# Optimization experiments

Measured on AMD Instinct MI355X. Metric: run time of the kernel, lower is better.

## Reference

```python
import jax, jax.numpy as jnp
import numpy as np

N_NODES = 100000
N_EDGES = 1600000
D_IN, D_HID, D_OUT = 128, 128, 64


def setup_inputs() -> dict:
    key = jax.random.key(0)
    ks = jax.random.split(key, 6)
    x = jax.random.normal(ks[0], (N_NODES, D_IN), dtype=jnp.float32)
    edge_index = jax.random.randint(ks[1], (2, N_EDGES), 0, N_NODES, dtype=jnp.int64)
    s1 = 1.0 / np.sqrt(D_IN)
    s2 = 1.0 / np.sqrt(D_HID)
    return {
        "x": x,
        "edge_index": edge_index,
        "Wl1": jax.random.uniform(ks[2], (D_HID, D_IN), jnp.float32, -s1, s1),
        "bl1": jnp.zeros((D_HID,), jnp.float32),
        "Wr1": jax.random.uniform(ks[3], (D_HID, D_IN), jnp.float32, -s1, s1),
        "Wl2": jax.random.uniform(ks[4], (D_OUT, D_HID), jnp.float32, -s2, s2),
        "bl2": jnp.zeros((D_OUT,), jnp.float32),
        "Wr2": jax.random.uniform(ks[5], (D_OUT, D_HID), jnp.float32, -s2, s2),
    }


def _sage_conv(x, src, dst, Wl, bl, Wr, n_nodes):
    # mean-aggregate neighbor features src -> dst
    agg = jax.ops.segment_sum(x[src], dst, num_segments=n_nodes)  # [N, d_in]
    deg = jax.ops.segment_sum(jnp.ones((src.shape[0],), x.dtype), dst, num_segments=n_nodes)
    agg = agg / jnp.maximum(deg, 1.0)[:, None]
    # PyG SAGEConv: lin_l(agg) + lin_r(x), bias only on lin_l
    return agg @ Wl.T + bl + x @ Wr.T


def reference(x, edge_index, Wl1, bl1, Wr1, Wl2, bl2, Wr2):
    src, dst = edge_index[0], edge_index[1]
    n = x.shape[0]
    h = _sage_conv(x, src, dst, Wl1, bl1, Wr1, n)
    h = jax.nn.relu(h)
    # dropout is identity in eval mode (training=False)
    out = _sage_conv(h, src, dst, Wl2, bl2, Wr2, n)
    return out
```

## Files before the change

kernel.cpp:

```cpp
#include <hip/hip_runtime.h>

#define N_NODES_C 100000
#define N_EDGES_C 1600000
#define NT32_C 3125
#define NBUCK_C 392
#define BCAP_C 4800
#define EPB_C 2048

typedef _Float16 half_t;
typedef __attribute__((ext_vector_type(2))) _Float16 half2v;
typedef __attribute__((ext_vector_type(8))) _Float16 half8v;
typedef __attribute__((ext_vector_type(4))) float floatx4;

#if defined(__has_builtin)
#if __has_builtin(__builtin_amdgcn_fdot2)
#define HAS_FDOT2 1
#endif
#endif

__global__ void bucket_kernel(const int* __restrict__ src, const int* __restrict__ dst,
                              int* __restrict__ gcur, int* __restrict__ bucket, int E) {
    __shared__ int lcnt[NBUCK_C];
    __shared__ int lbase[NBUCK_C];
    __shared__ int lcur[NBUCK_C];
    const int tid = threadIdx.x;
    const int e0 = blockIdx.x * EPB_C;
    const int n = min(EPB_C, E - e0);

    for (int i = tid; i < NBUCK_C; i += 256) { lcnt[i] = 0; lcur[i] = 0; }
    __syncthreads();
    for (int i = tid; i < n; i += 256) {
        atomicAdd(&lcnt[dst[e0 + i] >> 8], 1);
    }
    __syncthreads();
    for (int i = tid; i < NBUCK_C; i += 256) {
        int c = lcnt[i];
        lbase[i] = (c > 0) ? atomicAdd(&gcur[i], c) : 0;
    }
    __syncthreads();
    for (int i = tid; i < n; i += 256) {
        int d = dst[e0 + i];
        int s = src[e0 + i];
        int b = d >> 8;
        int p = lbase[b] + atomicAdd(&lcur[b], 1);
        if (p < BCAP_C) bucket[b * BCAP_C + p] = (s << 8) | (d & 255);
    }
}

__global__ void csr_build_kernel(const int* __restrict__ gcur, const int* __restrict__ bucket,
                                 int2* __restrict__ nodeinfo, int* __restrict__ csr, int N) {
    __shared__ int sg[NBUCK_C];
    __shared__ int lcnt[256];
    __shared__ int lcur[256];
    __shared__ int sc[2][256];
    __shared__ int eord[BCAP_C];
    __shared__ int sbase_s;
    const int b = blockIdx.x;
    const int tid = threadIdx.x;
    const int ne = min(gcur[b], BCAP_C);

    for (int i = tid; i < NBUCK_C; i += 256) sg[i] = min(gcur[i], BCAP_C);
    lcnt[tid] = 0;
    lcur[tid] = 0;
    __syncthreads();
    if (tid == 0) {
        int s = 0;
        for (int i = 0; i < b; i++) s += sg[i];
        sbase_s = s;
    }
    const int* be = bucket + b * BCAP_C;
    for (int i = tid; i < ne; i += 256) {
        atomicAdd(&lcnt[be[i] & 255], 1);
    }
    __syncthreads();
    sc[0][tid] = lcnt[tid];
    __syncthreads();
    int cur = 0;
    for (int off = 1; off < 256; off <<= 1) {
        int v = sc[cur][tid] + ((tid >= off) ? sc[cur][tid - off] : 0);
        sc[1 - cur][tid] = v;
        __syncthreads();
        cur ^= 1;
    }
    for (int i = tid; i < ne; i += 256) {
        int p = be[i];
        int dl = p & 255;
        int slot = atomicAdd(&lcur[dl], 1);
        int pre = (dl == 0) ? 0 : sc[cur][dl - 1];
        eord[pre + slot] = p >> 8;
    }
    __syncthreads();
    const int sbase = sbase_s;
    for (int i = tid; i < ne; i += 256) csr[sbase + i] = eord[i];
    int node = (b << 8) + tid;
    if (node < N) {
        int pre = (tid == 0) ? 0 : sc[cur][tid - 1];
        nodeinfo[node] = make_int2(sbase + pre, lcnt[tid]);
    }
}

__global__ void prep_kernel(const float* __restrict__ Wl1, const float* __restrict__ Wr1,
                            const float* __restrict__ Wl2, const float* __restrict__ Wr2,
                            const float* __restrict__ x,
                            half_t* __restrict__ B1, half_t* __restrict__ B2,
                            half_t* __restrict__ xh) {
    int blk = blockIdx.x;
    int tid = threadIdx.x;
    if (blk < 128) {
        int t = blk * 256 + tid;
        int j  = t & 7;
        int l  = (t >> 3) & 63;
        int ks = (t >> 9) & 7;
        int ct = t >> 12;
        int k = ks * 32 + ((l >> 4) << 3) + j;
        int o = ct * 16 + (l & 15);
        float v = (k < 128) ? Wl1[o * 128 + k] : Wr1[o * 128 + (k - 128)];
        B1[t] = (half_t)v;
    } else if (blk < 192) {
        int t = (blk - 128) * 256 + tid;
        int j  = t & 7;
        int l  = (t >> 3) & 63;
        int ks = (t >> 9) & 3;
        int ct = t >> 11;
        int k = ks * 32 + ((l >> 4) << 3) + j;
        int o = ct * 16 + (l & 15);
        float v = (o < 64) ? Wl2[o * 128 + k] : Wr2[(o - 64) * 128 + k];
        B2[t] = (half_t)v;
    } else {
        int t = (blk - 192) * 256 + tid;
        if (t >= N_NODES_C * 16) return;
        const float4* p = (const float4*)x;
        float4 a = p[(size_t)t * 2];
        float4 b = p[(size_t)t * 2 + 1];
        half_t r[8] = {(half_t)a.x, (half_t)a.y, (half_t)a.z, (half_t)a.w,
                       (half_t)b.x, (half_t)b.y, (half_t)b.z, (half_t)b.w};
        *(uint4*)(xh + (size_t)t * 8) = *(uint4*)r;
    }
}

static __device__ __forceinline__ void dot8(float* a, uint4 v) {
    unsigned int u[4] = {v.x, v.y, v.z, v.w};
#ifdef HAS_FDOT2
    const half2v e0 = {(half_t)1.0f, (half_t)0.0f};
    const half2v e1 = {(half_t)0.0f, (half_t)1.0f};
#pragma unroll
    for (int i = 0; i < 4; i++) {
        union { unsigned int x; half2v h; } c; c.x = u[i];
        a[2 * i]     = __builtin_amdgcn_fdot2(c.h, e0, a[2 * i], false);
        a[2 * i + 1] = __builtin_amdgcn_fdot2(c.h, e1, a[2 * i + 1], false);
    }
#else
#pragma unroll
    for (int i = 0; i < 4; i++) {
        union { unsigned int x; half2v h; } c; c.x = u[i];
        a[2 * i]     += (float)c.h.x;
        a[2 * i + 1] += (float)c.h.y;
    }
#endif
}

__launch_bounds__(256, 2)
__global__ void l1_kernel(const half_t* __restrict__ xh,
                          const int2* __restrict__ nodeinfo,
                          const int* __restrict__ csr,
                          const half_t* __restrict__ B1,
                          const float* __restrict__ bias,
                          half_t* __restrict__ hh) {
    __shared__ half_t sA[32][264];

    const int wave = threadIdx.x >> 6;
    const int lane = threadIdx.x & 63;
    const int quad = lane >> 4;
    const int l16 = lane & 15;
    const int tid = threadIdx.x;
    const int node0 = blockIdx.x * 32;

    for (int u = tid; u < 512; u += 256) {
        int n = u >> 4, cc = u & 15;
        *(half8v*)&sA[n][128 + cc * 8] =
            *(const half8v*)(xh + (size_t)(node0 + n) * 128 + cc * 8);
    }

    for (int i = 0; i < 8; i++) {
        const int n = wave * 8 + i;
        const int2 info = nodeinfo[node0 + n];
        const int* row = csr + info.x;
        const int deg = info.y;
        float a0[8] = {0,0,0,0,0,0,0,0};
        float a1[8] = {0,0,0,0,0,0,0,0};
        int e = quad;
        for (; e + 4 < deg; e += 8) {
            int s0 = row[e];
            int s1 = row[e + 4];
            uint4 v0 = *(const uint4*)(xh + (size_t)s0 * 128 + l16 * 8);
            uint4 v1 = *(const uint4*)(xh + (size_t)s1 * 128 + l16 * 8);
            dot8(a0, v0);
            dot8(a1, v1);
        }
        if (e < deg) {
            uint4 v0 = *(const uint4*)(xh + (size_t)row[e] * 128 + l16 * 8);
            dot8(a0, v0);
        }
        float sc = 1.0f / fmaxf((float)deg, 1.0f);
#pragma unroll
        for (int j = 0; j < 8; j++) {
            float v = a0[j] + a1[j];
            v += __shfl_xor(v, 16, 64);
            v += __shfl_xor(v, 32, 64);
            a0[j] = v * sc;
        }
        if (lane < 16) {
            half_t r[8];
#pragma unroll
            for (int j = 0; j < 8; j++) r[j] = (half_t)a0[j];
            *(uint4*)&sA[n][l16 * 8] = *(uint4*)r;
        }
    }
    __syncthreads();

    half8v bf[2][8];
    float bias_v[2];
#pragma unroll
    for (int i = 0; i < 2; i++) {
        int ct = wave * 2 + i;
        bias_v[i] = bias[ct * 16 + l16];
#pragma unroll
        for (int ks = 0; ks < 8; ks++) {
            bf[i][ks] = *(const half8v*)(B1 + ((ct * 8 + ks) * 64 + lane) * 8);
        }
    }

    floatx4 acc[2][2];
#pragma unroll
    for (int i = 0; i < 2; i++)
#pragma unroll
        for (int s = 0; s < 2; s++)
            acc[i][s] = (floatx4){0.f, 0.f, 0.f, 0.f};

#pragma unroll
    for (int ks = 0; ks < 8; ks++) {
        half8v a0 = *(const half8v*)&sA[l16][ks * 32 + quad * 8];
        half8v a1 = *(const half8v*)&sA[16 + l16][ks * 32 + quad * 8];
#pragma unroll
        for (int i = 0; i < 2; i++) {
            acc[i][0] = __builtin_amdgcn_mfma_f32_16x16x32_f16(a0, bf[i][ks], acc[i][0], 0, 0, 0);
            acc[i][1] = __builtin_amdgcn_mfma_f32_16x16x32_f16(a1, bf[i][ks], acc[i][1], 0, 0, 0);
        }
    }

#pragma unroll
    for (int i = 0; i < 2; i++) {
        int o = wave * 32 + i * 16 + l16;
#pragma unroll
        for (int s = 0; s < 2; s++) {
            float vals[4] = {acc[i][s].x, acc[i][s].y, acc[i][s].z, acc[i][s].w};
#pragma unroll
            for (int r = 0; r < 4; r++) {
                int node = node0 + s * 16 + quad * 4 + r;
                float v = fmaxf(vals[r] + bias_v[i], 0.f);
                hh[(size_t)node * 128 + o] = (half_t)v;
            }
        }
    }
}

__launch_bounds__(256, 2)
__global__ void gemm2_kernel(const half_t* __restrict__ hh,
                             const half_t* __restrict__ B2,
                             const float* __restrict__ bias,
                             half_t* __restrict__ g,
                             half_t* __restrict__ s2h) {
    __shared__ half_t sA[32][136];

    const int wave = threadIdx.x >> 6;
    const int lane = threadIdx.x & 63;
    const int quad = lane >> 4;
    const int l16 = lane & 15;

    half8v bf[2][4];
    float bias_v[2];
#pragma unroll
    for (int i = 0; i < 2; i++) {
        int ct = wave * 2 + i;
        int o = ct * 16 + l16;
        bias_v[i] = (o >= 64) ? bias[o - 64] : 0.f;
#pragma unroll
        for (int ks = 0; ks < 4; ks++) {
            bf[i][ks] = *(const half8v*)(B2 + ((ct * 4 + ks) * 64 + lane) * 8);
        }
    }

    const int tid = threadIdx.x;

    for (int tile = blockIdx.x; tile < NT32_C; tile += gridDim.x) {
        const int node0 = tile * 32;
        for (int u = tid; u < 512; u += 256) {
            int n = u >> 4, cc = u & 15;
            *(half8v*)&sA[n][cc * 8] =
                *(const half8v*)(hh + (size_t)(node0 + n) * 128 + cc * 8);
        }
        __syncthreads();

        floatx4 acc[2][2];
#pragma unroll
        for (int i = 0; i < 2; i++)
#pragma unroll
            for (int s = 0; s < 2; s++)
                acc[i][s] = (floatx4){0.f, 0.f, 0.f, 0.f};

#pragma unroll
        for (int ks = 0; ks < 4; ks++) {
            half8v a0 = *(const half8v*)&sA[l16][ks * 32 + quad * 8];
            half8v a1 = *(const half8v*)&sA[16 + l16][ks * 32 + quad * 8];
#pragma unroll
            for (int i = 0; i < 2; i++) {
                acc[i][0] = __builtin_amdgcn_mfma_f32_16x16x32_f16(a0, bf[i][ks], acc[i][0], 0, 0, 0);
                acc[i][1] = __builtin_amdgcn_mfma_f32_16x16x32_f16(a1, bf[i][ks], acc[i][1], 0, 0, 0);
            }
        }

#pragma unroll
        for (int i = 0; i < 2; i++) {
            int o = wave * 32 + i * 16 + l16;
#pragma unroll
            for (int s = 0; s < 2; s++) {
                float vals[4] = {acc[i][s].x, acc[i][s].y, acc[i][s].z, acc[i][s].w};
#pragma unroll
                for (int r = 0; r < 4; r++) {
                    int node = node0 + s * 16 + quad * 4 + r;
                    float v = vals[r] + bias_v[i];
                    if (o < 64) g[(size_t)node * 64 + o] = (half_t)v;
                    else        s2h[(size_t)node * 64 + (o - 64)] = (half_t)v;
                }
            }
        }
        __syncthreads();
    }
}

__global__ void agg2e_kernel(const half_t* __restrict__ g,
                             const half_t* __restrict__ s2h,
                             const int2* __restrict__ nodeinfo,
                             const int* __restrict__ csr,
                             float* __restrict__ out, int N) {
    int wid = (blockIdx.x * 256 + threadIdx.x) >> 6;
    if (wid >= N) return;
    int lane = threadIdx.x & 63;
    int q = lane >> 3;
    int c = lane & 7;
    int2 info = nodeinfo[wid];
    const int* row = csr + info.x;
    const int deg = info.y;
    float a0[8] = {0,0,0,0,0,0,0,0};
    float a1[8] = {0,0,0,0,0,0,0,0};
    int e = q;
    for (; e + 8 < deg; e += 16) {
        int s0 = row[e];
        int s1 = row[e + 8];
        uint4 v0 = *(const uint4*)(g + (size_t)s0 * 64 + c * 8);
        uint4 v1 = *(const uint4*)(g + (size_t)s1 * 64 + c * 8);
        dot8(a0, v0);
        dot8(a1, v1);
    }
    if (e < deg) {
        uint4 v0 = *(const uint4*)(g + (size_t)row[e] * 64 + c * 8);
        dot8(a0, v0);
    }
    float acc[8];
#pragma unroll
    for (int j = 0; j < 8; j++) {
        float v = a0[j] + a1[j];
        v += __shfl_xor(v, 8, 64);
        v += __shfl_xor(v, 16, 64);
        v += __shfl_xor(v, 32, 64);
        acc[j] = v;
    }
    if (lane < 8) {
        float sc = 1.0f / fmaxf((float)deg, 1.0f);
        uint4 sv = *(const uint4*)(s2h + (size_t)wid * 64 + c * 8);
        union { unsigned int x; half2v h; } c0, c1, c2, c3;
        c0.x = sv.x; c1.x = sv.y; c2.x = sv.z; c3.x = sv.w;
        float4 r0, r1;
        r0.x = acc[0] * sc + (float)c0.h.x;
        r0.y = acc[1] * sc + (float)c0.h.y;
        r0.z = acc[2] * sc + (float)c1.h.x;
        r0.w = acc[3] * sc + (float)c1.h.y;
        r1.x = acc[4] * sc + (float)c2.h.x;
        r1.y = acc[5] * sc + (float)c2.h.y;
        r1.z = acc[6] * sc + (float)c3.h.x;
        r1.w = acc[7] * sc + (float)c3.h.y;
        *(float4*)(out + (size_t)wid * 64 + c * 8) = r0;
        *(float4*)(out + (size_t)wid * 64 + c * 8 + 4) = r1;
    }
}

extern "C" void kernel_launch(void* const* d_in, const int* in_sizes, int n_in,
                              void* d_out, int out_size, void* d_ws, size_t ws_size,
                              hipStream_t stream) {
    const float* x    = (const float*)d_in[0];
    const int*   ei   = (const int*)d_in[1];
    const float* Wl1  = (const float*)d_in[2];
    const float* bl1  = (const float*)d_in[3];
    const float* Wr1  = (const float*)d_in[4];
    const float* Wl2  = (const float*)d_in[5];
    const float* bl2  = (const float*)d_in[6];
    const float* Wr2  = (const float*)d_in[7];
    float* out = (float*)d_out;

    const int N = N_NODES_C;
    const int E = N_EDGES_C;
    const int* src = ei;
    const int* dst = ei + E;

    char* ws = (char*)d_ws;
    half_t* B1   = (half_t*)(ws + 0);
    half_t* B2   = (half_t*)(ws + 65536);
    int*    gcur = (int*)   (ws + 98304);
    int2*   nodeinfo = (int2*)(ws + 102400);
    int*    csr  = (int*)   (ws + 1048576);
    half_t* xh   = (half_t*)(ws + 7448576);
    half_t* aggh = (half_t*)(ws + 33048576);
    half_t* hh   = (half_t*)(ws + 58648576);
    half_t* g    = aggh;
    half_t* s2h  = aggh + 6400000;
    int*    bucket = (int*)hh;

    hipMemsetAsync(gcur, 0, NBUCK_C * sizeof(int), stream);
    bucket_kernel<<<(E + EPB_C - 1) / EPB_C, 256, 0, stream>>>(src, dst, gcur, bucket, E);
    csr_build_kernel<<<NBUCK_C, 256, 0, stream>>>(gcur, bucket, nodeinfo, csr, N);

    prep_kernel<<<192 + (N * 16 + 255) / 256, 256, 0, stream>>>(
        Wl1, Wr1, Wl2, Wr2, x, B1, B2, xh);

    l1_kernel<<<NT32_C, 256, 0, stream>>>(xh, nodeinfo, csr, B1, bl1, hh);

    gemm2_kernel<<<512, 256, 0, stream>>>(hh, B2, bl2, g, s2h);
    agg2e_kernel<<<(N + 3) / 4, 256, 0, stream>>>(g, s2h, nodeinfo, csr, out, N);
}
```

Before: 278.7 us.

## Replace bucketed CSR build with global degree count, scan, and atomic scatter

```diff
diff --git a/kernel.cpp b/kernel.cpp
--- a/kernel.cpp
+++ b/kernel.cpp
@@ -4,8 +4,6 @@
 #define N_EDGES_C 1600000
 #define NT32_C 3125
 #define NBUCK_C 392
-#define BCAP_C 4800
-#define EPB_C 2048
 
 typedef _Float16 half_t;
 typedef __attribute__((ext_vector_type(2))) _Float16 half2v;
@@ -18,84 +16,81 @@
 #endif
 #endif
 
-__global__ void bucket_kernel(const int* __restrict__ src, const int* __restrict__ dst,
-                              int* __restrict__ gcur, int* __restrict__ bucket, int E) {
-    __shared__ int lcnt[NBUCK_C];
-    __shared__ int lbase[NBUCK_C];
-    __shared__ int lcur[NBUCK_C];
-    const int tid = threadIdx.x;
-    const int e0 = blockIdx.x * EPB_C;
-    const int n = min(EPB_C, E - e0);
-
-    for (int i = tid; i < NBUCK_C; i += 256) { lcnt[i] = 0; lcur[i] = 0; }
-    __syncthreads();
-    for (int i = tid; i < n; i += 256) {
-        atomicAdd(&lcnt[dst[e0 + i] >> 8], 1);
-    }
-    __syncthreads();
-    for (int i = tid; i < NBUCK_C; i += 256) {
-        int c = lcnt[i];
-        lbase[i] = (c > 0) ? atomicAdd(&gcur[i], c) : 0;
-    }
-    __syncthreads();
-    for (int i = tid; i < n; i += 256) {
-        int d = dst[e0 + i];
-        int s = src[e0 + i];
-        int b = d >> 8;
-        int p = lbase[b] + atomicAdd(&lcur[b], 1);
-        if (p < BCAP_C) bucket[b * BCAP_C + p] = (s << 8) | (d & 255);
-    }
-}
-
-__global__ void csr_build_kernel(const int* __restrict__ gcur, const int* __restrict__ bucket,
-                                 int2* __restrict__ nodeinfo, int* __restrict__ csr, int N) {
-    __shared__ int sg[NBUCK_C];
-    __shared__ int lcnt[256];
-    __shared__ int lcur[256];
+__global__ void deg_kernel(const int* __restrict__ dst, int* __restrict__ deg, int E4) {
+    int t = blockIdx.x * 256 + threadIdx.x;
+    if (t >= E4) return;
+    int4 d = ((const int4*)dst)[t];
+    atomicAdd(&deg[d.x], 1);
+    atomicAdd(&deg[d.y], 1);
+    atomicAdd(&deg[d.z], 1);
+    atomicAdd(&deg[d.w], 1);
+}
+
+__global__ void scan1_kernel(const int* __restrict__ deg, int2* __restrict__ nodeinfo,
+                             int* __restrict__ btot, int N) {
     __shared__ int sc[2][256];
-    __shared__ int eord[BCAP_C];
-    __shared__ int sbase_s;
     const int b = blockIdx.x;
     const int tid = threadIdx.x;
-    const int ne = min(gcur[b], BCAP_C);
-
-    for (int i = tid; i < NBUCK_C; i += 256) sg[i] = min(gcur[i], BCAP_C);
-    lcnt[tid] = 0;
-    lcur[tid] = 0;
-    __syncthreads();
-    if (tid == 0) {
-        int s = 0;
-        for (int i = 0; i < b; i++) s += sg[i];
-        sbase_s = s;
-    }
-    const int* be = bucket + b * BCAP_C;
-    for (int i = tid; i < ne; i += 256) {
-        atomicAdd(&lcnt[be[i] & 255], 1);
-    }
-    __syncthreads();
-    sc[0][tid] = lcnt[tid];
+    const int node = b * 256 + tid;
+    int v = (node < N) ? deg[node] : 0;
+    sc[0][tid] = v;
     __syncthreads();
     int cur = 0;
     for (int off = 1; off < 256; off <<= 1) {
-        int v = sc[cur][tid] + ((tid >= off) ? sc[cur][tid - off] : 0);
-        sc[1 - cur][tid] = v;
+        int nv = sc[cur][tid] + ((tid >= off) ? sc[cur][tid - off] : 0);
+        sc[1 - cur][tid] = nv;
         __syncthreads();
         cur ^= 1;
     }
-    for (int i = tid; i < ne; i += 256) {
-        int p = be[i];
-        int dl = p & 255;
-        int slot = atomicAdd(&lcur[dl], 1);
-        int pre = (dl == 0) ? 0 : sc[cur][dl - 1];
-        eord[pre + slot] = p >> 8;
-    }
+    int incl = sc[cur][tid];
+    if (node < N) nodeinfo[node] = make_int2(incl - v, v);
+    if (tid == 255) btot[b] = incl;
+}
+
+__global__ void scan2_kernel(const int* __restrict__ btot, int* __restrict__ bbase) {
+    __shared__ int sc[2][512];
+    const int tid = threadIdx.x;
+    int v = (tid < NBUCK_C) ? btot[tid] : 0;
+    sc[0][tid] = v;
     __syncthreads();
-    const int sbase = sbase_s;
-    for (int i = tid; i < ne; i += 256) csr[sbase + i] = eord[i];
-    int node = (b << 8) + tid;
-    if (node < N) {
-        int pre = (tid == 0) ? 0 : sc[cur][tid - 1];
-        nodeinfo[node] = make_int2(sbase + pre, lcnt[tid]);
+    int cur = 0;
+    for (int off = 1; off < 512; off <<= 1) {
+        int nv = sc[cur][tid] + ((tid >= off) ? sc[cur][tid - off] : 0);
+        sc[1 - cur][tid] = nv;
+        __syncthreads();
+        cur ^= 1;
+    }
+    if (tid < NBUCK_C) bbase[tid] = sc[cur][tid] - v;
+}
+
+__global__ void fix_kernel(int2* __restrict__ nodeinfo, const int* __restrict__ bbase, int N) {
+    const int b = blockIdx.x;
+    const int node = b * 256 + threadIdx.x;
+    if (node < N) nodeinfo[node].x += bbase[b];
+}
+
+__global__ void scatter_kernel(const int* __restrict__ src, const int* __restrict__ dst,
+                               const int2* __restrict__ nodeinfo, int* __restrict__ cur,
+                               int* __restrict__ csr, int E4) {
+    int t = blockIdx.x * 256 + threadIdx.x;
+    if (t >= E4) return;
+    int4 s = ((const int4*)src)[t];
+    int4 d = ((const int4*)dst)[t];
+    {
+        int p = atomicAdd(&cur[d.x], 1);
+        csr[nodeinfo[d.x].x + p] = s.x;
+    }
+    {
+        int p = atomicAdd(&cur[d.y], 1);
+        csr[nodeinfo[d.y].x + p] = s.y;
+    }
+    {
+        int p = atomicAdd(&cur[d.z], 1);
+        csr[nodeinfo[d.z].x + p] = s.z;
+    }
+    {
+        int p = atomicAdd(&cur[d.w], 1);
+        csr[nodeinfo[d.w].x + p] = s.w;
     }
 }
 
@@ -415,7 +410,8 @@
     char* ws = (char*)d_ws;
     half_t* B1   = (half_t*)(ws + 0);
     half_t* B2   = (half_t*)(ws + 65536);
-    int*    gcur = (int*)   (ws + 98304);
+    int*    btot = (int*)   (ws + 98304);
+    int*    bbase= (int*)   (ws + 100352);
     int2*   nodeinfo = (int2*)(ws + 102400);
     int*    csr  = (int*)   (ws + 1048576);
     half_t* xh   = (half_t*)(ws + 7448576);
@@ -423,11 +419,17 @@
     half_t* hh   = (half_t*)(ws + 58648576);
     half_t* g    = aggh;
     half_t* s2h  = aggh + 6400000;
-    int*    bucket = (int*)hh;
-
-    hipMemsetAsync(gcur, 0, NBUCK_C * sizeof(int), stream);
-    bucket_kernel<<<(E + EPB_C - 1) / EPB_C, 256, 0, stream>>>(src, dst, gcur, bucket, E);
-    csr_build_kernel<<<NBUCK_C, 256, 0, stream>>>(gcur, bucket, nodeinfo, csr, N);
+    int*    deg  = (int*)hh;
+    int*    curp = deg + 100352;
+
+    const int E4 = E / 4;
+
+    hipMemsetAsync(deg, 0, 2 * 100352 * sizeof(int), stream);
+    deg_kernel<<<(E4 + 255) / 256, 256, 0, stream>>>(dst, deg, E4);
+    scan1_kernel<<<NBUCK_C, 256, 0, stream>>>(deg, nodeinfo, btot, N);
+    scan2_kernel<<<1, 512, 0, stream>>>(btot, bbase);
+    fix_kernel<<<NBUCK_C, 256, 0, stream>>>(nodeinfo, bbase, N);
+    scatter_kernel<<<(E4 + 255) / 256, 256, 0, stream>>>(src, dst, nodeinfo, curp, csr, E4);
 
     prep_kernel<<<192 + (N * 16 + 255) / 256, 256, 0, stream>>>(
         Wl1, Wr1, Wl2, Wr2, x, B1, B2, xh);
```

Result: slower. 396.7 us (+42.3%).

## Sort edges locally before bucket scatter and split CSR build across four blocks per bucket

Applied to the files above, without the earlier changes.

```diff
diff --git a/kernel.cpp b/kernel.cpp
--- a/kernel.cpp
+++ b/kernel.cpp
@@ -6,6 +6,7 @@
 #define NBUCK_C 392
 #define BCAP_C 4800
 #define EPB_C 2048
+#define EORD_CAP_C 1536
 
 typedef _Float16 half_t;
 typedef __attribute__((ext_vector_type(2))) _Float16 half2v;
@@ -18,59 +19,100 @@
 #endif
 #endif
 
+__launch_bounds__(512, 1)
 __global__ void bucket_kernel(const int* __restrict__ src, const int* __restrict__ dst,
                               int* __restrict__ gcur, int* __restrict__ bucket, int E) {
-    __shared__ int lcnt[NBUCK_C];
-    __shared__ int lbase[NBUCK_C];
-    __shared__ int lcur[NBUCK_C];
+    __shared__ int stage[EPB_C];
+    __shared__ unsigned short ebkt[EPB_C];
+    __shared__ int eord[EPB_C];
+    __shared__ unsigned short obkt[EPB_C];
+    __shared__ int lcnt[512];
+    __shared__ int lcur[512];
+    __shared__ int lbase[512];
+    __shared__ int sc[2][512];
     const int tid = threadIdx.x;
     const int e0 = blockIdx.x * EPB_C;
     const int n = min(EPB_C, E - e0);
 
-    for (int i = tid; i < NBUCK_C; i += 256) { lcnt[i] = 0; lcur[i] = 0; }
-    __syncthreads();
-    for (int i = tid; i < n; i += 256) {
-        atomicAdd(&lcnt[dst[e0 + i] >> 8], 1);
-    }
-    __syncthreads();
-    for (int i = tid; i < NBUCK_C; i += 256) {
-        int c = lcnt[i];
-        lbase[i] = (c > 0) ? atomicAdd(&gcur[i], c) : 0;
-    }
-    __syncthreads();
-    for (int i = tid; i < n; i += 256) {
+    lcnt[tid] = 0;
+    lcur[tid] = 0;
+    __syncthreads();
+    for (int i = tid; i < n; i += 512) {
         int d = dst[e0 + i];
         int s = src[e0 + i];
         int b = d >> 8;
-        int p = lbase[b] + atomicAdd(&lcur[b], 1);
-        if (p < BCAP_C) bucket[b * BCAP_C + p] = (s << 8) | (d & 255);
-    }
-}
-
-__global__ void csr_build_kernel(const int* __restrict__ gcur, const int* __restrict__ bucket,
+        stage[i] = (s << 8) | (d & 255);
+        ebkt[i] = (unsigned short)b;
+        atomicAdd(&lcnt[b], 1);
+    }
+    __syncthreads();
+    sc[0][tid] = lcnt[tid];
+    __syncthreads();
+    int cur = 0;
+    for (int off = 1; off < 512; off <<= 1) {
+        int v = sc[cur][tid] + ((tid >= off) ? sc[cur][tid - off] : 0);
+        sc[1 - cur][tid] = v;
+        __syncthreads();
+        cur ^= 1;
+    }
+    for (int i = tid; i < NBUCK_C; i += 512) {
+        int c = lcnt[i];
+        lbase[i] = (c > 0) ? atomicAdd(&gcur[i], c) : 0;
+    }
+    __syncthreads();
+    for (int i = tid; i < n; i += 512) {
+        int b = ebkt[i];
+        int slot = atomicAdd(&lcur[b], 1);
+        int pos = (sc[cur][b] - lcnt[b]) + slot;
+        eord[pos] = stage[i];
+        obkt[pos] = (unsigned short)b;
+    }
+    __syncthreads();
+    for (int i = tid; i < n; i += 512) {
+        int b = obkt[i];
+        int pre = sc[cur][b] - lcnt[b];
+        int gpos = lbase[b] + (i - pre);
+        if (gpos < BCAP_C) bucket[b * BCAP_C + gpos] = eord[i];
+    }
+}
+
+__global__ void scanb_kernel(const int* __restrict__ gcur, int* __restrict__ bbase) {
+    __shared__ int sc[2][512];
+    const int tid = threadIdx.x;
+    int v = (tid < NBUCK_C) ? min(gcur[tid], BCAP_C) : 0;
+    sc[0][tid] = v;
+    __syncthreads();
+    int cur = 0;
+    for (int off = 1; off < 512; off <<= 1) {
+        int nv = sc[cur][tid] + ((tid >= off) ? sc[cur][tid - off] : 0);
+        sc[1 - cur][tid] = nv;
+        __syncthreads();
+        cur ^= 1;
+    }
+    if (tid < NBUCK_C) bbase[tid] = sc[cur][tid] - v;
+}
+
+__global__ void csr_build_kernel(const int* __restrict__ gcur, const int* __restrict__ bbase,
+                                 const int* __restrict__ bucket,
                                  int2* __restrict__ nodeinfo, int* __restrict__ csr, int N) {
-    __shared__ int sg[NBUCK_C];
+    __shared__ int stage[BCAP_C];
     __shared__ int lcnt[256];
-    __shared__ int lcur[256];
+    __shared__ int lcur[64];
     __shared__ int sc[2][256];
-    __shared__ int eord[BCAP_C];
-    __shared__ int sbase_s;
-    const int b = blockIdx.x;
+    __shared__ int eord[EORD_CAP_C];
+    const int b = blockIdx.x >> 2;
+    const int r = blockIdx.x & 3;
     const int tid = threadIdx.x;
     const int ne = min(gcur[b], BCAP_C);
 
-    for (int i = tid; i < NBUCK_C; i += 256) sg[i] = min(gcur[i], BCAP_C);
     lcnt[tid] = 0;
-    lcur[tid] = 0;
-    __syncthreads();
-    if (tid == 0) {
-        int s = 0;
-        for (int i = 0; i < b; i++) s += sg[i];
-        sbase_s = s;
-    }
+    if (tid < 64) lcur[tid] = 0;
     const int* be = bucket + b * BCAP_C;
+    __syncthreads();
     for (int i = tid; i < ne; i += 256) {
-        atomicAdd(&lcnt[be[i] & 255], 1);
+        int p = be[i];
+        stage[i] = p;
+        atomicAdd(&lcnt[p & 255], 1);
     }
     __syncthreads();
     sc[0][tid] = lcnt[tid];
@@ -82,20 +124,27 @@
         __syncthreads();
         cur ^= 1;
     }
+    const int j0 = r * 64;
+    const int pre0 = (j0 == 0) ? 0 : sc[cur][j0 - 1];
+    const int L = min(sc[cur][j0 + 63] - pre0, EORD_CAP_C);
     for (int i = tid; i < ne; i += 256) {
-        int p = be[i];
-        int dl = p & 255;
-        int slot = atomicAdd(&lcur[dl], 1);
-        int pre = (dl == 0) ? 0 : sc[cur][dl - 1];
-        eord[pre + slot] = p >> 8;
-    }
-    __syncthreads();
-    const int sbase = sbase_s;
-    for (int i = tid; i < ne; i += 256) csr[sbase + i] = eord[i];
-    int node = (b << 8) + tid;
-    if (node < N) {
-        int pre = (tid == 0) ? 0 : sc[cur][tid - 1];
-        nodeinfo[node] = make_int2(sbase + pre, lcnt[tid]);
+        int p = stage[i];
+        int j = p & 255;
+        if ((j >> 6) == r) {
+            int slot = atomicAdd(&lcur[j - j0], 1);
+            int idx = (sc[cur][j] - lcnt[j]) - pre0 + slot;
+            if (idx < EORD_CAP_C) eord[idx] = p >> 8;
+        }
+    }
+    __syncthreads();
+    const int gb = bbase[b] + pre0;
+    for (int i = tid; i < L; i += 256) csr[gb + i] = eord[i];
+    if (tid < 64) {
+        int node = (b << 8) + j0 + tid;
+        if (node < N) {
+            int j = j0 + tid;
+            nodeinfo[node] = make_int2(bbase[b] + (sc[cur][j] - lcnt[j]), lcnt[j]);
+        }
     }
 }
 
@@ -416,6 +465,7 @@
     half_t* B1   = (half_t*)(ws + 0);
     half_t* B2   = (half_t*)(ws + 65536);
     int*    gcur = (int*)   (ws + 98304);
+    int*    bbase= (int*)   (ws + 100352);
     int2*   nodeinfo = (int2*)(ws + 102400);
     int*    csr  = (int*)   (ws + 1048576);
     half_t* xh   = (half_t*)(ws + 7448576);
@@ -426,8 +476,9 @@
     int*    bucket = (int*)hh;
 
     hipMemsetAsync(gcur, 0, NBUCK_C * sizeof(int), stream);
-    bucket_kernel<<<(E + EPB_C - 1) / EPB_C, 256, 0, stream>>>(src, dst, gcur, bucket, E);
-    csr_build_kernel<<<NBUCK_C, 256, 0, stream>>>(gcur, bucket, nodeinfo, csr, N);
+    bucket_kernel<<<(E + EPB_C - 1) / EPB_C, 512, 0, stream>>>(src, dst, gcur, bucket, E);
+    scanb_kernel<<<1, 512, 0, stream>>>(gcur, bbase);
+    csr_build_kernel<<<NBUCK_C * 4, 256, 0, stream>>>(gcur, bbase, bucket, nodeinfo, csr, N);
 
     prep_kernel<<<192 + (N * 16 + 255) / 256, 256, 0, stream>>>(
         Wl1, Wr1, Wl2, Wr2, x, B1, B2, xh);
```

Measured after the change: 278.5 us. Within noise of the previous version (-0.1%).
